# Performance work log

Measured on AMD Instinct MI355X. Metric: run time of the kernel, lower is better.

## Reference

```python
import jax, jax.numpy as jnp
import numpy as np

# Fixed_pool: four depthwise 2x2 stride-2 convs with one-hot filters.
# Filter k (row-major over the 2x2 window) selects pixel (k//2, k%2) of each
# 2x2 block, i.e. the op is exactly a pixel-unshuffle / strided subsample:
#   LL = x[:, :, 0::2, 0::2]
#   LH = x[:, :, 0::2, 1::2]
#   HL = x[:, :, 1::2, 0::2]
#   HH = x[:, :, 1::2, 1::2]

def setup_inputs() -> dict:
    key = jax.random.key(0)
    x = jax.random.normal(key, (8, 256, 256, 256), dtype=jnp.float32)  # NCHW
    return {"x": x}

def reference(x):
    ll = x[:, :, 0::2, 0::2]
    lh = x[:, :, 0::2, 1::2]
    hl = x[:, :, 1::2, 0::2]
    hh = x[:, :, 1::2, 1::2]
    return (ll, lh, hl, hh)
```

## Files before the change

kernel.cpp:

```cpp
#include <hip/hip_runtime.h>


typedef float f32x4 __attribute__((ext_vector_type(4)));
typedef float f32x2 __attribute__((ext_vector_type(2)));

__global__ __launch_bounds__(256) void deinterleave2x2_kernel(
    const f32x4* __restrict__ in,
    float* __restrict__ out,
    size_t nitems,
    size_t outsz)
{
    const size_t stride = (size_t)gridDim.x * blockDim.x;
    for (size_t t = (size_t)blockIdx.x * blockDim.x + threadIdx.x;
         t < nitems; t += stride) {
        const size_t l   = t & 63;
        const size_t p   = t >> 6;
        const size_t hp  = p & 127;
        const size_t img = p >> 7;

        const f32x4 e = __builtin_nontemporal_load(&in[128 * p + l]);
        const f32x4 o = __builtin_nontemporal_load(&in[128 * p + 64 + l]);

        const size_t off = img * (size_t)(128 * 128) + hp * 128 + 2 * l;

        f32x2 ll; ll.x = e.x; ll.y = e.z;
        f32x2 lh; lh.x = e.y; lh.y = e.w;
        f32x2 hl; hl.x = o.x; hl.y = o.z;
        f32x2 hh; hh.x = o.y; hh.y = o.w;

        __builtin_nontemporal_store(ll, reinterpret_cast<f32x2*>(out + off));
        __builtin_nontemporal_store(lh, reinterpret_cast<f32x2*>(out + outsz + off));
        __builtin_nontemporal_store(hl, reinterpret_cast<f32x2*>(out + 2 * outsz + off));
        __builtin_nontemporal_store(hh, reinterpret_cast<f32x2*>(out + 3 * outsz + off));
    }
}

extern "C" void kernel_launch(void* const* d_in, const int* in_sizes, int n_in,
                              void* d_out, int out_size, void* d_ws, size_t ws_size,
                              hipStream_t stream) {
    const float* x = (const float*)d_in[0];
    float* out = (float*)d_out;

    const size_t total  = (size_t)in_sizes[0];
    const size_t nitems = total >> 3;
    const size_t outsz  = total >> 2;

    const int threads = 256;
    const int blocks  = 2048;

    deinterleave2x2_kernel<<<blocks, threads, 0, stream>>>(
        reinterpret_cast<const f32x4*>(x), out, nitems, outsz);
}
```

Baseline: 194.8 us.

## Use DPP lane swaps to write 16-byte output vectors per thread

Each thread now handles two row pairs (four float4 loads). Adjacent lanes exchange elements through DPP quad-permute swaps, so every lane writes a full float4 to a single output plane instead of four float2 stores across four planes. The goal is wider, fully coalesced stores and more loads in flight per thread. The cost is extra select and DPP instructions, and the input loads are no longer marked nontemporal.

```diff
diff --git a/kernel.cpp b/kernel.cpp
--- a/kernel.cpp
+++ b/kernel.cpp
@@ -2,7 +2,11 @@
 
 
 typedef float f32x4 __attribute__((ext_vector_type(4)));
-typedef float f32x2 __attribute__((ext_vector_type(2)));
+
+__device__ __forceinline__ float dpp_swap_adj(float x) {
+    return __int_as_float(__builtin_amdgcn_update_dpp(
+        0, __float_as_int(x), 0xB1, 0xF, 0xF, true));
+}
 
 __global__ __launch_bounds__(256) void deinterleave2x2_kernel(
     const f32x4* __restrict__ in,
@@ -13,25 +17,41 @@
     const size_t stride = (size_t)gridDim.x * blockDim.x;
     for (size_t t = (size_t)blockIdx.x * blockDim.x + threadIdx.x;
          t < nitems; t += stride) {
-        const size_t l   = t & 63;
-        const size_t p   = t >> 6;
-        const size_t hp  = p & 127;
-        const size_t img = p >> 7;
+        const int    l   = (int)(t & 63);
+        const size_t g   = t >> 6;
+        const size_t rp  = (g & 63) * 2;
+        const size_t img = g >> 6;
 
-        const f32x4 e = __builtin_nontemporal_load(&in[128 * p + l]);
-        const f32x4 o = __builtin_nontemporal_load(&in[128 * p + 64 + l]);
+        const size_t ib = 256 * g + l;
+        const f32x4 v0 = in[ib];
+        const f32x4 v1 = in[ib + 64];
+        const f32x4 v2 = in[ib + 128];
+        const f32x4 v3 = in[ib + 192];
 
-        const size_t off = img * (size_t)(128 * 128) + hp * 128 + 2 * l;
+        const bool evl = (l & 1) == 0;
+        const int  j   = l >> 1;
 
-        f32x2 ll; ll.x = e.x; ll.y = e.z;
-        f32x2 lh; lh.x = e.y; lh.y = e.w;
-        f32x2 hl; hl.x = o.x; hl.y = o.z;
-        f32x2 hh; hh.x = o.y; hh.y = o.w;
+        const size_t off = img * (size_t)(128 * 128) + rp * 128 + 4 * (size_t)j;
+        float* pA = out + (evl ? (size_t)0 : outsz) + off;
+        float* pB = pA + 2 * outsz;
 
-        __builtin_nontemporal_store(ll, reinterpret_cast<f32x2*>(out + off));
-        __builtin_nontemporal_store(lh, reinterpret_cast<f32x2*>(out + outsz + off));
-        __builtin_nontemporal_store(hl, reinterpret_cast<f32x2*>(out + 2 * outsz + off));
-        __builtin_nontemporal_store(hh, reinterpret_cast<f32x2*>(out + 3 * outsz + off));
+        auto proc = [&](f32x4 v, float* dst) {
+            float s0 = evl ? v.y : v.x;
+            float s1 = evl ? v.w : v.z;
+            float r0 = dpp_swap_adj(s0);
+            float r1 = dpp_swap_adj(s1);
+            f32x4 res;
+            res.x = evl ? v.x : r0;
+            res.y = evl ? v.z : r1;
+            res.z = evl ? r0 : v.y;
+            res.w = evl ? r1 : v.w;
+            __builtin_nontemporal_store(res, reinterpret_cast<f32x4*>(dst));
+        };
+
+        proc(v0, pA);
+        proc(v1, pB);
+        proc(v2, pA + 128);
+        proc(v3, pB + 128);
     }
 }
 
@@ -42,7 +62,7 @@
     float* out = (float*)d_out;
 
     const size_t total  = (size_t)in_sizes[0];
-    const size_t nitems = total >> 3;
+    const size_t nitems = total >> 4;
     const size_t outsz  = total >> 2;
 
     const int threads = 256;
```

New measurement: 197.3 us. Within noise of the previous version (+1.3%).

## Stage row pairs through swizzled LDS to emit 16-byte output stores

Applied to the files above, without the earlier changes.

Each wavefront now loads two input row pairs (four 16-byte loads per thread) into a private, XOR-swizzled LDS region. It then reads the data back rearranged so every thread writes full 16-byte float4 stores to each of the four outputs instead of 8-byte stores. The aim is wider, more efficient write transactions and more bytes in flight per thread. The cost is LDS traffic, and loads are no longer nontemporal. No barrier is used because each wave owns its own LDS slice, which relies on wavefront-synchronous execution within the 64-lane wave.

```diff
diff --git a/kernel.cpp b/kernel.cpp
--- a/kernel.cpp
+++ b/kernel.cpp
@@ -2,7 +2,8 @@
 
 
 typedef float f32x4 __attribute__((ext_vector_type(4)));
-typedef float f32x2 __attribute__((ext_vector_type(2)));
+
+__device__ __forceinline__ int swz(int i) { return i ^ ((i >> 3) & 7); }
 
 __global__ __launch_bounds__(256) void deinterleave2x2_kernel(
     const f32x4* __restrict__ in,
@@ -10,28 +11,47 @@
     size_t nitems,
     size_t outsz)
 {
+    __shared__ f32x4 lds[4 * 256];
+    const int tid = (int)threadIdx.x;
+    const int l   = tid & 63;
+    const int m   = l & 31;
+    const int h   = l >> 5;
+    f32x4* wl = &lds[(tid >> 6) * 256];
+
     const size_t stride = (size_t)gridDim.x * blockDim.x;
     for (size_t t = (size_t)blockIdx.x * blockDim.x + threadIdx.x;
          t < nitems; t += stride) {
-        const size_t l   = t & 63;
-        const size_t p   = t >> 6;
-        const size_t hp  = p & 127;
-        const size_t img = p >> 7;
+        const size_t g   = t >> 6;
+        const size_t img = g >> 6;
+        const size_t G2  = (g & 63) * 2;
 
-        const f32x4 e = __builtin_nontemporal_load(&in[128 * p + l]);
-        const f32x4 o = __builtin_nontemporal_load(&in[128 * p + 64 + l]);
+        const size_t ib = 256 * g;
+        const f32x4 v0 = in[ib + l];
+        const f32x4 v1 = in[ib + 64 + l];
+        const f32x4 v2 = in[ib + 128 + l];
+        const f32x4 v3 = in[ib + 192 + l];
 
-        const size_t off = img * (size_t)(128 * 128) + hp * 128 + 2 * l;
+        wl[swz(l)]       = v0;
+        wl[swz(64 + l)]  = v1;
+        wl[swz(128 + l)] = v2;
+        wl[swz(192 + l)] = v3;
 
-        f32x2 ll; ll.x = e.x; ll.y = e.z;
-        f32x2 lh; lh.x = e.y; lh.y = e.w;
-        f32x2 hl; hl.x = o.x; hl.y = o.z;
-        f32x2 hh; hh.x = o.y; hh.y = o.w;
+        const f32x4 A0 = wl[swz(128 * h + 2 * m)];
+        const f32x4 A1 = wl[swz(128 * h + 2 * m + 1)];
+        const f32x4 B0 = wl[swz(128 * h + 64 + 2 * m)];
+        const f32x4 B1 = wl[swz(128 * h + 64 + 2 * m + 1)];
 
-        __builtin_nontemporal_store(ll, reinterpret_cast<f32x2*>(out + off));
-        __builtin_nontemporal_store(lh, reinterpret_cast<f32x2*>(out + outsz + off));
-        __builtin_nontemporal_store(hl, reinterpret_cast<f32x2*>(out + 2 * outsz + off));
-        __builtin_nontemporal_store(hh, reinterpret_cast<f32x2*>(out + 3 * outsz + off));
+        f32x4 ll; ll.x = A0.x; ll.y = A0.z; ll.z = A1.x; ll.w = A1.z;
+        f32x4 lh; lh.x = A0.y; lh.y = A0.w; lh.z = A1.y; lh.w = A1.w;
+        f32x4 hl; hl.x = B0.x; hl.y = B0.z; hl.z = B1.x; hl.w = B1.z;
+        f32x4 hh; hh.x = B0.y; hh.y = B0.w; hh.z = B1.y; hh.w = B1.w;
+
+        const size_t off = img * (size_t)(128 * 128) + (G2 + h) * 128 + 4 * (size_t)m;
+
+        __builtin_nontemporal_store(ll, reinterpret_cast<f32x4*>(out + off));
+        __builtin_nontemporal_store(lh, reinterpret_cast<f32x4*>(out + outsz + off));
+        __builtin_nontemporal_store(hl, reinterpret_cast<f32x4*>(out + 2 * outsz + off));
+        __builtin_nontemporal_store(hh, reinterpret_cast<f32x4*>(out + 3 * outsz + off));
     }
 }
 
@@ -42,7 +62,7 @@
     float* out = (float*)d_out;
 
     const size_t total  = (size_t)in_sizes[0];
-    const size_t nitems = total >> 3;
+    const size_t nitems = total >> 4;
     const size_t outsz  = total >> 2;
 
     const int threads = 256;
```

After: 196.9 us. About the same (+1.1%).
